# Performance work log

Measured on AMD Instinct MI355X. Metric: run time of the kernel, lower is better.

## Reference

```python
import jax, jax.numpy as jnp
import numpy as np

TAU = 0.2
EPS_NORM = 1e-12  # torch F.normalize eps


def _l2_normalize(x):
    n = jnp.linalg.norm(x, axis=-1, keepdims=True)
    return x / jnp.maximum(n, EPS_NORM)


def setup_inputs() -> dict:
    key = jax.random.key(0)
    k1, k2 = jax.random.split(key)
    seg_emb = jax.random.normal(k1, (131072, 512), dtype=jnp.float32)
    prototypes = jax.random.normal(k2, (64, 512), dtype=jnp.float32) * 0.02
    return {"seg_emb": seg_emb, "prototypes": prototypes}


def reference(seg_emb, prototypes):
    # normalize -> cosine-sim matmul -> temperature scale -> softmax -> weighted proto sum
    p = _l2_normalize(prototypes)          # [K, D]
    z = _l2_normalize(seg_emb)             # [N, D]
    logits = jnp.einsum('nd,kd->nk', z, p) / max(TAU, 1e-06)  # [N, K]
    w = jax.nn.softmax(logits, axis=-1)    # [N, K]
    pattern = jnp.einsum('nk,kd->nd', w, prototypes)           # [N, D]
    return pattern, w, logits
```

## Files before the change

kernel.cpp:

```cpp
#include <hip/hip_runtime.h>
#include <hip/hip_bf16.h>

typedef __attribute__((ext_vector_type(8))) short short8;
typedef __attribute__((ext_vector_type(4))) float f32x4;

#define NPROTO 64
#define DIM    512
#define TAU_INV 5.0f

__device__ __forceinline__ unsigned short f2bf(float f) {
    union { float f; unsigned int u; } v; v.f = f;
    unsigned int r = v.u + 0x7FFFu + ((v.u >> 16) & 1u);
    return (unsigned short)(r >> 16);
}

__global__ void pb_prep(const float* __restrict__ protos,
                        unsigned short* __restrict__ pnorm,
                        unsigned short* __restrict__ protosT) {
    const int k    = blockIdx.x;
    const int lane = threadIdx.x;
    const float* row = protos + k * DIM;
    float x[8];
    float ss = 0.0f;
#pragma unroll
    for (int j = 0; j < 8; ++j) {
        x[j] = row[lane * 8 + j];
        ss += x[j] * x[j];
    }
#pragma unroll
    for (int m = 1; m < 64; m <<= 1) ss += __shfl_xor(ss, m, 64);
    const float s = 1.0f / fmaxf(sqrtf(ss), 1e-12f);
    short8 pn;
#pragma unroll
    for (int j = 0; j < 8; ++j) pn[j] = (short)f2bf(x[j] * s);
    *reinterpret_cast<short8*>(pnorm + k * DIM + lane * 8) = pn;
#pragma unroll
    for (int j = 0; j < 8; ++j)
        protosT[(lane * 8 + j) * NPROTO + k] = f2bf(x[j]);
}

__global__ __launch_bounds__(256) void pb_main(
    const float* __restrict__ seg,
    const unsigned short* __restrict__ pnorm,
    const unsigned short* __restrict__ protosT,
    float* __restrict__ out_pat,
    float* __restrict__ out_w,
    float* __restrict__ out_log) {

    __shared__ unsigned short wbuf_all[4 * 16 * 64];

    const int wid  = (int)(threadIdx.x >> 6);
    const int lane = (int)(threadIdx.x & 63);
    const int g    = lane >> 4;
    const int r16  = lane & 15;
    const long n0  = ((long)blockIdx.x * 4 + wid) * 16;

    f32x4 acc[4] = {};
    float ss = 0.0f;
    const float* aptr = seg + (n0 + r16) * DIM + g * 8;
#pragma unroll 4
    for (int kt = 0; kt < 16; ++kt) {
        const f32x4 a0 = *reinterpret_cast<const f32x4*>(aptr + kt * 32);
        const f32x4 a1 = *reinterpret_cast<const f32x4*>(aptr + kt * 32 + 4);
        short8 af;
#pragma unroll
        for (int j = 0; j < 4; ++j) {
            ss += a0[j] * a0[j];
            ss += a1[j] * a1[j];
            af[j]     = (short)f2bf(a0[j]);
            af[j + 4] = (short)f2bf(a1[j]);
        }
#pragma unroll
        for (int c = 0; c < 4; ++c) {
            const short8 bf = *reinterpret_cast<const short8*>(
                pnorm + (c * 16 + r16) * DIM + g * 8 + kt * 32);
            acc[c] = __builtin_amdgcn_mfma_f32_16x16x32_bf16(af, bf, acc[c], 0, 0, 0);
        }
    }

    ss += __shfl_xor(ss, 16, 64);
    ss += __shfl_xor(ss, 32, 64);
    const float sc_own = TAU_INV / fmaxf(sqrtf(ss), 1e-12f);
    float sc[4];
#pragma unroll
    for (int q = 0; q < 4; ++q) sc[q] = __shfl(sc_own, g * 4 + q, 64);

    float lg[4][4];
#pragma unroll
    for (int c = 0; c < 4; ++c)
#pragma unroll
        for (int q = 0; q < 4; ++q) {
            lg[c][q] = acc[c][q] * sc[q];
            out_log[(n0 + g * 4 + q) * NPROTO + c * 16 + r16] = lg[c][q];
        }

    float w[4][4];
#pragma unroll
    for (int q = 0; q < 4; ++q) {
        float mx = fmaxf(fmaxf(lg[0][q], lg[1][q]), fmaxf(lg[2][q], lg[3][q]));
#pragma unroll
        for (int msk = 1; msk < 16; msk <<= 1) mx = fmaxf(mx, __shfl_xor(mx, msk, 64));
        const float e0 = __expf(lg[0][q] - mx);
        const float e1 = __expf(lg[1][q] - mx);
        const float e2 = __expf(lg[2][q] - mx);
        const float e3 = __expf(lg[3][q] - mx);
        float sum = e0 + e1 + e2 + e3;
#pragma unroll
        for (int msk = 1; msk < 16; msk <<= 1) sum += __shfl_xor(sum, msk, 64);
        const float inv = 1.0f / sum;
        w[0][q] = e0 * inv; w[1][q] = e1 * inv; w[2][q] = e2 * inv; w[3][q] = e3 * inv;
    }

    unsigned short* wb = wbuf_all + wid * (16 * 64);
#pragma unroll
    for (int c = 0; c < 4; ++c)
#pragma unroll
        for (int q = 0; q < 4; ++q) {
            out_w[(n0 + g * 4 + q) * NPROTO + c * 16 + r16] = w[c][q];
            const int row  = g * 4 + q;
            const int col  = c * 16 + r16;
            const int byte = (row * 128 + col * 2) ^ ((row & 7) << 4);
            *reinterpret_cast<unsigned short*>(reinterpret_cast<char*>(wb) + byte) =
                f2bf(w[c][q]);
        }

    __syncthreads();

    short8 wa0, wa1;
    {
        const int row = r16;
        const int b0 = (row * 128 + g * 16)      ^ ((row & 7) << 4);
        const int b1 = (row * 128 + g * 16 + 64) ^ ((row & 7) << 4);
        wa0 = *reinterpret_cast<const short8*>(reinterpret_cast<char*>(wb) + b0);
        wa1 = *reinterpret_cast<const short8*>(reinterpret_cast<char*>(wb) + b1);
    }

#pragma unroll 2
    for (int cp = 0; cp < 32; ++cp) {
        const unsigned short* bp = protosT + (cp * 16 + r16) * NPROTO + g * 8;
        const short8 b0 = *reinterpret_cast<const short8*>(bp);
        const short8 b1 = *reinterpret_cast<const short8*>(bp + 32);
        f32x4 pacc = {};
        pacc = __builtin_amdgcn_mfma_f32_16x16x32_bf16(wa0, b0, pacc, 0, 0, 0);
        pacc = __builtin_amdgcn_mfma_f32_16x16x32_bf16(wa1, b1, pacc, 0, 0, 0);
#pragma unroll
        for (int q = 0; q < 4; ++q)
            out_pat[(n0 + g * 4 + q) * DIM + cp * 16 + r16] = pacc[q];
    }
}

extern "C" void kernel_launch(void* const* d_in, const int* in_sizes, int n_in,
                              void* d_out, int out_size, void* d_ws, size_t ws_size,
                              hipStream_t stream) {
    const float* seg    = (const float*)d_in[0];
    const float* protos = (const float*)d_in[1];
    const int N = in_sizes[0] / DIM;

    float* out     = (float*)d_out;
    float* out_pat = out;
    float* out_w   = out_pat + (size_t)N * DIM;
    float* out_log = out_w + (size_t)N * NPROTO;

    unsigned short* pnorm   = (unsigned short*)d_ws;
    unsigned short* protosT = pnorm + NPROTO * DIM;

    pb_prep<<<NPROTO, 64, 0, stream>>>(protos, pnorm, protosT);
    pb_main<<<N / 64, 256, 0, stream>>>(seg, pnorm, protosT, out_pat, out_w, out_log);
}
```

Baseline: 200.2 us.

## Process two 16-row tiles per wave and software-prefetch activation loads

Each wave now handles 32 rows instead of 16, so every prototype B-fragment load (pnorm and protosT) is reused across two MFMA tiles, and the grid is halved. The K-loop is fully unrolled and the next iteration's fp32 activation loads are issued before the current tile's conversion and MFMAs, to hide global-memory latency. Launch bounds are raised to request 4 blocks per CU. The cost is higher register pressure and twice the LDS per block, which could limit occupancy. The kernel is memory-bound on roughly 256MB of input plus output, so the gain is likely limited.

```diff
diff --git a/kernel.cpp b/kernel.cpp
--- a/kernel.cpp
+++ b/kernel.cpp
@@ -39,7 +39,7 @@
         protosT[(lane * 8 + j) * NPROTO + k] = f2bf(x[j]);
 }
 
-__global__ __launch_bounds__(256) void pb_main(
+__global__ __launch_bounds__(256, 4) void pb_main(
     const float* __restrict__ seg,
     const unsigned short* __restrict__ pnorm,
     const unsigned short* __restrict__ protosT,
@@ -47,92 +47,125 @@
     float* __restrict__ out_w,
     float* __restrict__ out_log) {
 
-    __shared__ unsigned short wbuf_all[4 * 16 * 64];
+    __shared__ unsigned short wbuf_all[4 * 2 * 16 * 64];
 
     const int wid  = (int)(threadIdx.x >> 6);
     const int lane = (int)(threadIdx.x & 63);
     const int g    = lane >> 4;
     const int r16  = lane & 15;
-    const long n0  = ((long)blockIdx.x * 4 + wid) * 16;
-
-    f32x4 acc[4] = {};
-    float ss = 0.0f;
-    const float* aptr = seg + (n0 + r16) * DIM + g * 8;
-#pragma unroll 4
+    const long n0  = ((long)blockIdx.x * 4 + wid) * 32;
+
+    f32x4 acc0[4] = {}, acc1[4] = {};
+    float ss0 = 0.0f, ss1 = 0.0f;
+    const float* ap0 = seg + (n0 + r16) * DIM + g * 8;
+    const float* ap1 = ap0 + 16 * DIM;
+
+    f32x4 a00 = *reinterpret_cast<const f32x4*>(ap0);
+    f32x4 a01 = *reinterpret_cast<const f32x4*>(ap0 + 4);
+    f32x4 a10 = *reinterpret_cast<const f32x4*>(ap1);
+    f32x4 a11 = *reinterpret_cast<const f32x4*>(ap1 + 4);
+
+#pragma unroll
     for (int kt = 0; kt < 16; ++kt) {
-        const f32x4 a0 = *reinterpret_cast<const f32x4*>(aptr + kt * 32);
-        const f32x4 a1 = *reinterpret_cast<const f32x4*>(aptr + kt * 32 + 4);
-        short8 af;
+        f32x4 n00, n01, n10, n11;
+        if (kt < 15) {
+            n00 = *reinterpret_cast<const f32x4*>(ap0 + (kt + 1) * 32);
+            n01 = *reinterpret_cast<const f32x4*>(ap0 + (kt + 1) * 32 + 4);
+            n10 = *reinterpret_cast<const f32x4*>(ap1 + (kt + 1) * 32);
+            n11 = *reinterpret_cast<const f32x4*>(ap1 + (kt + 1) * 32 + 4);
+        }
+        short8 af0, af1;
 #pragma unroll
         for (int j = 0; j < 4; ++j) {
-            ss += a0[j] * a0[j];
-            ss += a1[j] * a1[j];
-            af[j]     = (short)f2bf(a0[j]);
-            af[j + 4] = (short)f2bf(a1[j]);
-        }
+            ss0 += a00[j] * a00[j] + a01[j] * a01[j];
+            ss1 += a10[j] * a10[j] + a11[j] * a11[j];
+            af0[j] = (short)f2bf(a00[j]); af0[j + 4] = (short)f2bf(a01[j]);
+            af1[j] = (short)f2bf(a10[j]); af1[j + 4] = (short)f2bf(a11[j]);
+        }
+        const unsigned short* bbase = pnorm + r16 * DIM + g * 8 + kt * 32;
 #pragma unroll
         for (int c = 0; c < 4; ++c) {
-            const short8 bf = *reinterpret_cast<const short8*>(
-                pnorm + (c * 16 + r16) * DIM + g * 8 + kt * 32);
-            acc[c] = __builtin_amdgcn_mfma_f32_16x16x32_bf16(af, bf, acc[c], 0, 0, 0);
-        }
-    }
-
-    ss += __shfl_xor(ss, 16, 64);
-    ss += __shfl_xor(ss, 32, 64);
-    const float sc_own = TAU_INV / fmaxf(sqrtf(ss), 1e-12f);
-    float sc[4];
-#pragma unroll
-    for (int q = 0; q < 4; ++q) sc[q] = __shfl(sc_own, g * 4 + q, 64);
-
-    float lg[4][4];
+            const short8 bf = *reinterpret_cast<const short8*>(bbase + c * 16 * DIM);
+            acc0[c] = __builtin_amdgcn_mfma_f32_16x16x32_bf16(af0, bf, acc0[c], 0, 0, 0);
+            acc1[c] = __builtin_amdgcn_mfma_f32_16x16x32_bf16(af1, bf, acc1[c], 0, 0, 0);
+        }
+        if (kt < 15) { a00 = n00; a01 = n01; a10 = n10; a11 = n11; }
+    }
+
+    ss0 += __shfl_xor(ss0, 16, 64); ss0 += __shfl_xor(ss0, 32, 64);
+    ss1 += __shfl_xor(ss1, 16, 64); ss1 += __shfl_xor(ss1, 32, 64);
+    const float sco0 = TAU_INV / fmaxf(sqrtf(ss0), 1e-12f);
+    const float sco1 = TAU_INV / fmaxf(sqrtf(ss1), 1e-12f);
+    float sc0[4], sc1[4];
+#pragma unroll
+    for (int q = 0; q < 4; ++q) {
+        sc0[q] = __shfl(sco0, g * 4 + q, 64);
+        sc1[q] = __shfl(sco1, g * 4 + q, 64);
+    }
+
+    float lg0[4][4], lg1[4][4];
 #pragma unroll
     for (int c = 0; c < 4; ++c)
 #pragma unroll
         for (int q = 0; q < 4; ++q) {
-            lg[c][q] = acc[c][q] * sc[q];
-            out_log[(n0 + g * 4 + q) * NPROTO + c * 16 + r16] = lg[c][q];
-        }
-
-    float w[4][4];
+            lg0[c][q] = acc0[c][q] * sc0[q];
+            lg1[c][q] = acc1[c][q] * sc1[q];
+            out_log[(n0 + g * 4 + q) * NPROTO + c * 16 + r16]      = lg0[c][q];
+            out_log[(n0 + 16 + g * 4 + q) * NPROTO + c * 16 + r16] = lg1[c][q];
+        }
+
+    float w0[4][4], w1[4][4];
 #pragma unroll
     for (int q = 0; q < 4; ++q) {
-        float mx = fmaxf(fmaxf(lg[0][q], lg[1][q]), fmaxf(lg[2][q], lg[3][q]));
-#pragma unroll
-        for (int msk = 1; msk < 16; msk <<= 1) mx = fmaxf(mx, __shfl_xor(mx, msk, 64));
-        const float e0 = __expf(lg[0][q] - mx);
-        const float e1 = __expf(lg[1][q] - mx);
-        const float e2 = __expf(lg[2][q] - mx);
-        const float e3 = __expf(lg[3][q] - mx);
-        float sum = e0 + e1 + e2 + e3;
-#pragma unroll
-        for (int msk = 1; msk < 16; msk <<= 1) sum += __shfl_xor(sum, msk, 64);
-        const float inv = 1.0f / sum;
-        w[0][q] = e0 * inv; w[1][q] = e1 * inv; w[2][q] = e2 * inv; w[3][q] = e3 * inv;
-    }
-
-    unsigned short* wb = wbuf_all + wid * (16 * 64);
+        float mx0 = fmaxf(fmaxf(lg0[0][q], lg0[1][q]), fmaxf(lg0[2][q], lg0[3][q]));
+        float mx1 = fmaxf(fmaxf(lg1[0][q], lg1[1][q]), fmaxf(lg1[2][q], lg1[3][q]));
+#pragma unroll
+        for (int msk = 1; msk < 16; msk <<= 1) {
+            mx0 = fmaxf(mx0, __shfl_xor(mx0, msk, 64));
+            mx1 = fmaxf(mx1, __shfl_xor(mx1, msk, 64));
+        }
+        float e0[4], e1[4], sum0 = 0.0f, sum1 = 0.0f;
+#pragma unroll
+        for (int c = 0; c < 4; ++c) {
+            e0[c] = __expf(lg0[c][q] - mx0); sum0 += e0[c];
+            e1[c] = __expf(lg1[c][q] - mx1); sum1 += e1[c];
+        }
+#pragma unroll
+        for (int msk = 1; msk < 16; msk <<= 1) {
+            sum0 += __shfl_xor(sum0, msk, 64);
+            sum1 += __shfl_xor(sum1, msk, 64);
+        }
+        const float i0 = 1.0f / sum0, i1 = 1.0f / sum1;
+#pragma unroll
+        for (int c = 0; c < 4; ++c) { w0[c][q] = e0[c] * i0; w1[c][q] = e1[c] * i1; }
+    }
+
+    unsigned short* wb0 = wbuf_all + (wid * 2 + 0) * (16 * 64);
+    unsigned short* wb1 = wbuf_all + (wid * 2 + 1) * (16 * 64);
 #pragma unroll
     for (int c = 0; c < 4; ++c)
 #pragma unroll
         for (int q = 0; q < 4; ++q) {
-            out_w[(n0 + g * 4 + q) * NPROTO + c * 16 + r16] = w[c][q];
+            out_w[(n0 + g * 4 + q) * NPROTO + c * 16 + r16]      = w0[c][q];
+            out_w[(n0 + 16 + g * 4 + q) * NPROTO + c * 16 + r16] = w1[c][q];
             const int row  = g * 4 + q;
             const int col  = c * 16 + r16;
             const int byte = (row * 128 + col * 2) ^ ((row & 7) << 4);
-            *reinterpret_cast<unsigned short*>(reinterpret_cast<char*>(wb) + byte) =
-                f2bf(w[c][q]);
+            *reinterpret_cast<unsigned short*>(reinterpret_cast<char*>(wb0) + byte) = f2bf(w0[c][q]);
+            *reinterpret_cast<unsigned short*>(reinterpret_cast<char*>(wb1) + byte) = f2bf(w1[c][q]);
         }
 
     __syncthreads();
 
-    short8 wa0, wa1;
+    short8 wa[2][2];
     {
         const int row = r16;
         const int b0 = (row * 128 + g * 16)      ^ ((row & 7) << 4);
         const int b1 = (row * 128 + g * 16 + 64) ^ ((row & 7) << 4);
-        wa0 = *reinterpret_cast<const short8*>(reinterpret_cast<char*>(wb) + b0);
-        wa1 = *reinterpret_cast<const short8*>(reinterpret_cast<char*>(wb) + b1);
+        wa[0][0] = *reinterpret_cast<const short8*>(reinterpret_cast<char*>(wb0) + b0);
+        wa[0][1] = *reinterpret_cast<const short8*>(reinterpret_cast<char*>(wb0) + b1);
+        wa[1][0] = *reinterpret_cast<const short8*>(reinterpret_cast<char*>(wb1) + b0);
+        wa[1][1] = *reinterpret_cast<const short8*>(reinterpret_cast<char*>(wb1) + b1);
     }
 
 #pragma unroll 2
@@ -140,12 +173,16 @@
         const unsigned short* bp = protosT + (cp * 16 + r16) * NPROTO + g * 8;
         const short8 b0 = *reinterpret_cast<const short8*>(bp);
         const short8 b1 = *reinterpret_cast<const short8*>(bp + 32);
-        f32x4 pacc = {};
-        pacc = __builtin_amdgcn_mfma_f32_16x16x32_bf16(wa0, b0, pacc, 0, 0, 0);
-        pacc = __builtin_amdgcn_mfma_f32_16x16x32_bf16(wa1, b1, pacc, 0, 0, 0);
-#pragma unroll
-        for (int q = 0; q < 4; ++q)
-            out_pat[(n0 + g * 4 + q) * DIM + cp * 16 + r16] = pacc[q];
+        f32x4 p0 = {}, p1 = {};
+        p0 = __builtin_amdgcn_mfma_f32_16x16x32_bf16(wa[0][0], b0, p0, 0, 0, 0);
+        p0 = __builtin_amdgcn_mfma_f32_16x16x32_bf16(wa[0][1], b1, p0, 0, 0, 0);
+        p1 = __builtin_amdgcn_mfma_f32_16x16x32_bf16(wa[1][0], b0, p1, 0, 0, 0);
+        p1 = __builtin_amdgcn_mfma_f32_16x16x32_bf16(wa[1][1], b1, p1, 0, 0, 0);
+#pragma unroll
+        for (int q = 0; q < 4; ++q) {
+            out_pat[(n0 + g * 4 + q) * DIM + cp * 16 + r16]      = p0[q];
+            out_pat[(n0 + 16 + g * 4 + q) * DIM + cp * 16 + r16] = p1[q];
+        }
     }
 }
 
@@ -165,5 +202,5 @@
     unsigned short* protosT = pnorm + NPROTO * DIM;
 
     pb_prep<<<NPROTO, 64, 0, stream>>>(protos, pnorm, protosT);
-    pb_main<<<N / 64, 256, 0, stream>>>(seg, pnorm, protosT, out_pat, out_w, out_log);
-}
+    pb_main<<<N / 128, 256, 0, stream>>>(seg, pnorm, protosT, out_pat, out_w, out_log);
+}
```

After: 167.6 us. 1.19x faster.

## Stage embeddings through LDS with coalesced loads and prefetch prototype tiles

Applied to the files above, without the earlier changes.

Embedding rows are now loaded as fully coalesced row-contiguous float4 vectors with a one-chunk register prefetch. They are converted to bf16 and written into a swizzled per-wave LDS tile, from which the MFMA A-fragments are read. Row norms are computed by shuffle reductions during staging. The second GEMM double-buffers prototype fragments in registers, the block-wide barrier is dropped in favour of per-wave LDS regions, and launch bounds request 4 blocks per CU. This adds LDS traffic and more shuffles, and LDS use rises to 32KB per block.

```diff
diff --git a/kernel.cpp b/kernel.cpp
--- a/kernel.cpp
+++ b/kernel.cpp
@@ -39,7 +39,7 @@
         protosT[(lane * 8 + j) * NPROTO + k] = f2bf(x[j]);
 }
 
-__global__ __launch_bounds__(256) void pb_main(
+__global__ __launch_bounds__(256, 4) void pb_main(
     const float* __restrict__ seg,
     const unsigned short* __restrict__ pnorm,
     const unsigned short* __restrict__ protosT,
@@ -47,7 +47,7 @@
     float* __restrict__ out_w,
     float* __restrict__ out_log) {
 
-    __shared__ unsigned short wbuf_all[4 * 16 * 64];
+    __shared__ unsigned short lds_all[4 * 16 * 256];
 
     const int wid  = (int)(threadIdx.x >> 6);
     const int lane = (int)(threadIdx.x & 63);
@@ -55,32 +55,61 @@
     const int r16  = lane & 15;
     const long n0  = ((long)blockIdx.x * 4 + wid) * 16;
 
+    char* wlds = reinterpret_cast<char*>(lds_all + wid * 16 * 256);
+
     f32x4 acc[4] = {};
-    float ss = 0.0f;
-    const float* aptr = seg + (n0 + r16) * DIM + g * 8;
-#pragma unroll 4
-    for (int kt = 0; kt < 16; ++kt) {
-        const f32x4 a0 = *reinterpret_cast<const f32x4*>(aptr + kt * 32);
-        const f32x4 a1 = *reinterpret_cast<const f32x4*>(aptr + kt * 32 + 4);
-        short8 af;
+    float ss_own = 0.0f;
+    const int wr_slot = (lane >> 1) & 31;
+
+    for (int h = 0; h < 2; ++h) {
+        const float* sp = seg + n0 * DIM + h * 256 + lane * 4;
+        f32x4 v[4];
 #pragma unroll
-        for (int j = 0; j < 4; ++j) {
-            ss += a0[j] * a0[j];
-            ss += a1[j] * a1[j];
-            af[j]     = (short)f2bf(a0[j]);
-            af[j + 4] = (short)f2bf(a1[j]);
+        for (int i = 0; i < 4; ++i)
+            v[i] = *reinterpret_cast<const f32x4*>(sp + i * DIM);
+#pragma unroll
+        for (int ch = 0; ch < 4; ++ch) {
+            f32x4 nv[4];
+            if (ch < 3) {
+#pragma unroll
+                for (int i = 0; i < 4; ++i)
+                    nv[i] = *reinterpret_cast<const f32x4*>(sp + ((ch + 1) * 4 + i) * DIM);
+            }
+#pragma unroll
+            for (int i = 0; i < 4; ++i) {
+                const int row = ch * 4 + i;
+                float part = v[i][0] * v[i][0] + v[i][1] * v[i][1]
+                           + v[i][2] * v[i][2] + v[i][3] * v[i][3];
+                part += __shfl_xor(part, 1, 64);
+                part += __shfl_xor(part, 2, 64);
+                part += __shfl_xor(part, 4, 64);
+                part += __shfl_xor(part, 8, 64);
+                if (r16 == row) ss_own += part;
+                union { unsigned short s[4]; unsigned long long u; } pk;
+#pragma unroll
+                for (int j = 0; j < 4; ++j) pk.s[j] = f2bf(v[i][j]);
+                const int byte = row * 512 + ((wr_slot ^ (row & 7)) << 4) + ((lane & 1) << 3);
+                *reinterpret_cast<unsigned long long*>(wlds + byte) = pk.u;
+            }
+            if (ch < 3) { v[0] = nv[0]; v[1] = nv[1]; v[2] = nv[2]; v[3] = nv[3]; }
         }
 #pragma unroll
-        for (int c = 0; c < 4; ++c) {
-            const short8 bf = *reinterpret_cast<const short8*>(
-                pnorm + (c * 16 + r16) * DIM + g * 8 + kt * 32);
-            acc[c] = __builtin_amdgcn_mfma_f32_16x16x32_bf16(af, bf, acc[c], 0, 0, 0);
+        for (int kk = 0; kk < 8; ++kk) {
+            const int slot = (g + kk * 4) ^ (r16 & 7);
+            const short8 af = *reinterpret_cast<const short8*>(wlds + r16 * 512 + slot * 16);
+            const int kt = h * 8 + kk;
+            const unsigned short* bbase = pnorm + r16 * DIM + g * 8 + kt * 32;
+#pragma unroll
+            for (int c = 0; c < 4; ++c) {
+                const short8 bf = *reinterpret_cast<const short8*>(bbase + c * 16 * DIM);
+                acc[c] = __builtin_amdgcn_mfma_f32_16x16x32_bf16(af, bf, acc[c], 0, 0, 0);
+            }
         }
     }
 
-    ss += __shfl_xor(ss, 16, 64);
-    ss += __shfl_xor(ss, 32, 64);
-    const float sc_own = TAU_INV / fmaxf(sqrtf(ss), 1e-12f);
+    ss_own += __shfl_xor(ss_own, 16, 64);
+    ss_own += __shfl_xor(ss_own, 32, 64);
+    const float sc_own = TAU_INV / fmaxf(sqrtf(ss_own), 1e-12f);
     float sc[4];
 #pragma unroll
     for (int q = 0; q < 4; ++q) sc[q] = __shfl(sc_own, g * 4 + q, 64);
@@ -111,7 +140,6 @@
         w[0][q] = e0 * inv; w[1][q] = e1 * inv; w[2][q] = e2 * inv; w[3][q] = e3 * inv;
     }
 
-    unsigned short* wb = wbuf_all + wid * (16 * 64);
 #pragma unroll
     for (int c = 0; c < 4; ++c)
 #pragma unroll
@@ -120,32 +148,34 @@
             const int row  = g * 4 + q;
             const int col  = c * 16 + r16;
             const int byte = (row * 128 + col * 2) ^ ((row & 7) << 4);
-            *reinterpret_cast<unsigned short*>(reinterpret_cast<char*>(wb) + byte) =
-                f2bf(w[c][q]);
+            *reinterpret_cast<unsigned short*>(wlds + byte) = f2bf(w[c][q]);
         }
-
-    __syncthreads();
 
     short8 wa0, wa1;
     {
-        const int row = r16;
-        const int b0 = (row * 128 + g * 16)      ^ ((row & 7) << 4);
-        const int b1 = (row * 128 + g * 16 + 64) ^ ((row & 7) << 4);
-        wa0 = *reinterpret_cast<const short8*>(reinterpret_cast<char*>(wb) + b0);
-        wa1 = *reinterpret_cast<const short8*>(reinterpret_cast<char*>(wb) + b1);
+        const int b0 = (r16 * 128 + g * 16)      ^ ((r16 & 7) << 4);
+        const int b1 = (r16 * 128 + g * 16 + 64) ^ ((r16 & 7) << 4);
+        wa0 = *reinterpret_cast<const short8*>(wlds + b0);
+        wa1 = *reinterpret_cast<const short8*>(wlds + b1);
     }
 
-#pragma unroll 2
+    short8 pbuf[2][2];
+    const unsigned short* btile = protosT + r16 * NPROTO + g * 8;
+    pbuf[0][0] = *reinterpret_cast<const short8*>(btile);
+    pbuf[0][1] = *reinterpret_cast<const short8*>(btile + 32);
+#pragma unroll
     for (int cp = 0; cp < 32; ++cp) {
-        const unsigned short* bp = protosT + (cp * 16 + r16) * NPROTO + g * 8;
-        const short8 b0 = *reinterpret_cast<const short8*>(bp);
-        const short8 b1 = *reinterpret_cast<const short8*>(bp + 32);
-        f32x4 pacc = {};
-        pacc = __builtin_amdgcn_mfma_f32_16x16x32_bf16(wa0, b0, pacc, 0, 0, 0);
-        pacc = __builtin_amdgcn_mfma_f32_16x16x32_bf16(wa1, b1, pacc, 0, 0, 0);
+        if (cp < 31) {
+            const unsigned short* bn = btile + (cp + 1) * 16 * NPROTO;
+            pbuf[(cp + 1) & 1][0] = *reinterpret_cast<const short8*>(bn);
+            pbuf[(cp + 1) & 1][1] = *reinterpret_cast<const short8*>(bn + 32);
+        }
+        f32x4 p = {};
+        p = __builtin_amdgcn_mfma_f32_16x16x32_bf16(wa0, pbuf[cp & 1][0], p, 0, 0, 0);
+        p = __builtin_amdgcn_mfma_f32_16x16x32_bf16(wa1, pbuf[cp & 1][1], p, 0, 0, 0);
 #pragma unroll
         for (int q = 0; q < 4; ++q)
-            out_pat[(n0 + g * 4 + q) * DIM + cp * 16 + r16] = pacc[q];
+            out_pat[(n0 + g * 4 + q) * DIM + cp * 16 + r16] = p[q];
     }
 }
 
```

Result: no change. 200.8 us (+0.3%).

## Stage A and B tiles through LDS with async global_load_lds triple buffering

Applied to the files above, without the earlier changes.

The first GEMM now streams seg_emb and normalized prototype tiles into LDS with direct global-to-LDS loads, triple-buffered with manual vmcnt waits and barriers. The prototypes are pre-swizzled into a chunked layout in the prep kernel. The second GEMM double-buffers protosT register loads. Launch bounds are set to 2 blocks per CU. The aim is to hide global load latency. It costs about 72KB of LDS per block, which may limit occupancy, and adds two barriers per stage.

```diff
diff --git a/kernel.cpp b/kernel.cpp
--- a/kernel.cpp
+++ b/kernel.cpp
@@ -7,6 +7,9 @@
 #define NPROTO 64
 #define DIM    512
 #define TAU_INV 5.0f
+
+#define AS1 __attribute__((address_space(1)))
+#define AS3 __attribute__((address_space(3)))
 
 __device__ __forceinline__ unsigned short f2bf(float f) {
     union { float f; unsigned int u; } v; v.f = f;
@@ -15,7 +18,7 @@
 }
 
 __global__ void pb_prep(const float* __restrict__ protos,
-                        unsigned short* __restrict__ pnorm,
+                        unsigned short* __restrict__ pn2,
                         unsigned short* __restrict__ protosT) {
     const int k    = blockIdx.x;
     const int lane = threadIdx.x;
@@ -33,21 +36,25 @@
     short8 pn;
 #pragma unroll
     for (int j = 0; j < 8; ++j) pn[j] = (short)f2bf(x[j] * s);
-    *reinterpret_cast<short8*>(pnorm + k * DIM + lane * 8) = pn;
+    const int chunk = lane >> 3;
+    const int physg = (lane & 7) ^ (k & 7);
+    *reinterpret_cast<short8*>(pn2 + chunk * 4096 + k * 64 + physg * 8) = pn;
 #pragma unroll
     for (int j = 0; j < 8; ++j)
         protosT[(lane * 8 + j) * NPROTO + k] = f2bf(x[j]);
 }
 
-__global__ __launch_bounds__(256) void pb_main(
+__global__ __launch_bounds__(256, 2) void pb_main(
     const float* __restrict__ seg,
-    const unsigned short* __restrict__ pnorm,
+    const unsigned short* __restrict__ pn2,
     const unsigned short* __restrict__ protosT,
     float* __restrict__ out_pat,
     float* __restrict__ out_w,
     float* __restrict__ out_log) {
 
-    __shared__ unsigned short wbuf_all[4 * 16 * 64];
+    __shared__ char abuf[3][4][4096];
+    __shared__ char bbuf[3][8192];
+    __shared__ unsigned short wbuf_all[4 * 1024];
 
     const int wid  = (int)(threadIdx.x >> 6);
     const int lane = (int)(threadIdx.x & 63);
@@ -55,28 +62,73 @@
     const int r16  = lane & 15;
     const long n0  = ((long)blockIdx.x * 4 + wid) * 16;
 
+    const float* srcA[4];
+#pragma unroll
+    for (int j = 0; j < 4; ++j) {
+        const int row = j * 4 + (lane >> 4);
+        const int lg  = (lane & 15) ^ (row & 15);
+        srcA[j] = seg + (n0 + row) * DIM + lg * 4;
+    }
+
+#define STAGE(T) do {                                                          \
+    char* _da = &abuf[(T) % 3][wid][0];                                        \
+    _Pragma("unroll")                                                          \
+    for (int _j = 0; _j < 4; ++_j)                                             \
+        __builtin_amdgcn_global_load_lds(                                      \
+            (const AS1 void*)(srcA[_j] + (T) * 64),                            \
+            (AS3 void*)(_da + _j * 1024), 16, 0, 0);                           \
+    char* _db = &bbuf[(T) % 3][wid * 2048];                                    \
+    const unsigned short* _sb = pn2 + (T) * 4096 + wid * 1024 + lane * 8;      \
+    _Pragma("unroll")                                                          \
+    for (int _q = 0; _q < 2; ++_q)                                             \
+        __builtin_amdgcn_global_load_lds(                                      \
+            (const AS1 void*)(_sb + _q * 512),                                 \
+            (AS3 void*)(_db + _q * 1024), 16, 0, 0);                           \
+} while (0)
+
     f32x4 acc[4] = {};
     float ss = 0.0f;
-    const float* aptr = seg + (n0 + r16) * DIM + g * 8;
-#pragma unroll 4
-    for (int kt = 0; kt < 16; ++kt) {
-        const f32x4 a0 = *reinterpret_cast<const f32x4*>(aptr + kt * 32);
-        const f32x4 a1 = *reinterpret_cast<const f32x4*>(aptr + kt * 32 + 4);
-        short8 af;
-#pragma unroll
-        for (int j = 0; j < 4; ++j) {
-            ss += a0[j] * a0[j];
-            ss += a1[j] * a1[j];
-            af[j]     = (short)f2bf(a0[j]);
-            af[j + 4] = (short)f2bf(a1[j]);
-        }
-#pragma unroll
-        for (int c = 0; c < 4; ++c) {
-            const short8 bf = *reinterpret_cast<const short8*>(
-                pnorm + (c * 16 + r16) * DIM + g * 8 + kt * 32);
-            acc[c] = __builtin_amdgcn_mfma_f32_16x16x32_bf16(af, bf, acc[c], 0, 0, 0);
-        }
-    }
+
+    STAGE(0); STAGE(1); STAGE(2);
+
+#pragma unroll
+    for (int t = 0; t < 8; ++t) {
+        if (t <= 5)      asm volatile("s_waitcnt vmcnt(12)" ::: "memory");
+        else if (t == 6) asm volatile("s_waitcnt vmcnt(6)"  ::: "memory");
+        else             asm volatile("s_waitcnt vmcnt(0)"  ::: "memory");
+        __builtin_amdgcn_sched_barrier(0);
+        __builtin_amdgcn_s_barrier();
+        __builtin_amdgcn_sched_barrier(0);
+
+        const char* ab = &abuf[t % 3][wid][0];
+        const char* bb = &bbuf[t % 3][0];
+#pragma unroll
+        for (int kk = 0; kk < 2; ++kk) {
+            const int lga = (kk * 4 + g) * 2;
+            const f32x4 a0 = *reinterpret_cast<const f32x4*>(
+                ab + r16 * 256 + (((lga + 0) ^ r16) << 4));
+            const f32x4 a1 = *reinterpret_cast<const f32x4*>(
+                ab + r16 * 256 + (((lga + 1) ^ r16) << 4));
+            short8 af;
+#pragma unroll
+            for (int j = 0; j < 4; ++j) {
+                ss += a0[j] * a0[j] + a1[j] * a1[j];
+                af[j]     = (short)f2bf(a0[j]);
+                af[j + 4] = (short)f2bf(a1[j]);
+            }
+#pragma unroll
+            for (int c = 0; c < 4; ++c) {
+                const short8 bf = *reinterpret_cast<const short8*>(
+                    bb + (c * 16 + r16) * 128 + (((kk * 4 + g) ^ (r16 & 7)) << 4));
+                acc[c] = __builtin_amdgcn_mfma_f32_16x16x32_bf16(af, bf, acc[c], 0, 0, 0);
+            }
+        }
+        asm volatile("s_waitcnt lgkmcnt(0)" ::: "memory");
+        __builtin_amdgcn_sched_barrier(0);
+        __builtin_amdgcn_s_barrier();
+        if (t <= 4) STAGE(t + 3);
+    }
+#undef STAGE
 
     ss += __shfl_xor(ss, 16, 64);
     ss += __shfl_xor(ss, 32, 64);
@@ -111,7 +163,7 @@
         w[0][q] = e0 * inv; w[1][q] = e1 * inv; w[2][q] = e2 * inv; w[3][q] = e3 * inv;
     }
 
-    unsigned short* wb = wbuf_all + wid * (16 * 64);
+    char* wb = reinterpret_cast<char*>(wbuf_all + wid * 1024);
 #pragma unroll
     for (int c = 0; c < 4; ++c)
 #pragma unroll
@@ -120,32 +172,34 @@
             const int row  = g * 4 + q;
             const int col  = c * 16 + r16;
             const int byte = (row * 128 + col * 2) ^ ((row & 7) << 4);
-            *reinterpret_cast<unsigned short*>(reinterpret_cast<char*>(wb) + byte) =
-                f2bf(w[c][q]);
-        }
-
-    __syncthreads();
+            *reinterpret_cast<unsigned short*>(wb + byte) = f2bf(w[c][q]);
+        }
 
     short8 wa0, wa1;
     {
-        const int row = r16;
-        const int b0 = (row * 128 + g * 16)      ^ ((row & 7) << 4);
-        const int b1 = (row * 128 + g * 16 + 64) ^ ((row & 7) << 4);
-        wa0 = *reinterpret_cast<const short8*>(reinterpret_cast<char*>(wb) + b0);
-        wa1 = *reinterpret_cast<const short8*>(reinterpret_cast<char*>(wb) + b1);
-    }
-
-#pragma unroll 2
+        const int b0 = (r16 * 128 + g * 16)      ^ ((r16 & 7) << 4);
+        const int b1 = (r16 * 128 + g * 16 + 64) ^ ((r16 & 7) << 4);
+        wa0 = *reinterpret_cast<const short8*>(wb + b0);
+        wa1 = *reinterpret_cast<const short8*>(wb + b1);
+    }
+
+    short8 pbuf[2][2];
+    const unsigned short* btile = protosT + r16 * NPROTO + g * 8;
+    pbuf[0][0] = *reinterpret_cast<const short8*>(btile);
+    pbuf[0][1] = *reinterpret_cast<const short8*>(btile + 32);
+#pragma unroll
     for (int cp = 0; cp < 32; ++cp) {
-        const unsigned short* bp = protosT + (cp * 16 + r16) * NPROTO + g * 8;
-        const short8 b0 = *reinterpret_cast<const short8*>(bp);
-        const short8 b1 = *reinterpret_cast<const short8*>(bp + 32);
-        f32x4 pacc = {};
-        pacc = __builtin_amdgcn_mfma_f32_16x16x32_bf16(wa0, b0, pacc, 0, 0, 0);
-        pacc = __builtin_amdgcn_mfma_f32_16x16x32_bf16(wa1, b1, pacc, 0, 0, 0);
+        if (cp < 31) {
+            const unsigned short* bn = btile + (cp + 1) * 16 * NPROTO;
+            pbuf[(cp + 1) & 1][0] = *reinterpret_cast<const short8*>(bn);
+            pbuf[(cp + 1) & 1][1] = *reinterpret_cast<const short8*>(bn + 32);
+        }
+        f32x4 p = {};
+        p = __builtin_amdgcn_mfma_f32_16x16x32_bf16(wa0, pbuf[cp & 1][0], p, 0, 0, 0);
+        p = __builtin_amdgcn_mfma_f32_16x16x32_bf16(wa1, pbuf[cp & 1][1], p, 0, 0, 0);
 #pragma unroll
         for (int q = 0; q < 4; ++q)
-            out_pat[(n0 + g * 4 + q) * DIM + cp * 16 + r16] = pacc[q];
+            out_pat[(n0 + g * 4 + q) * DIM + cp * 16 + r16] = p[q];
     }
 }
 
@@ -161,9 +215,9 @@
     float* out_w   = out_pat + (size_t)N * DIM;
     float* out_log = out_w + (size_t)N * NPROTO;
 
-    unsigned short* pnorm   = (unsigned short*)d_ws;
-    unsigned short* protosT = pnorm + NPROTO * DIM;
-
-    pb_prep<<<NPROTO, 64, 0, stream>>>(protos, pnorm, protosT);
-    pb_main<<<N / 64, 256, 0, stream>>>(seg, pnorm, protosT, out_pat, out_w, out_log);
-}
+    unsigned short* pn2     = (unsigned short*)d_ws;
+    unsigned short* protosT = pn2 + 8 * 64 * 64;
+
+    pb_prep<<<NPROTO, 64, 0, stream>>>(protos, pn2, protosT);
+    pb_main<<<N / 64, 256, 0, stream>>>(seg, pn2, protosT, out_pat, out_w, out_log);
+}
```

After: 171.1 us. 1.17x faster.
